# Kernel tuning notes

Measured on AMD Instinct MI355X. Metric: run time of the kernel, lower is better.

Reference implementation:

```python
import jax, jax.numpy as jnp
import numpy as np

N = 50000
E = 800000
T = 12
HID = 128
K = 3
F_IN = 7  # 1 (x) + 4 (env) + 2 (coords)
CIN = F_IN + HID  # DCRNN concatenates input with hidden state


def setup_inputs() -> dict:
    key = jax.random.key(0)
    ks = jax.random.split(key, 16)
    inp = {
        "x": jax.random.normal(ks[0], (N, T), dtype=jnp.float32),
        "env": jax.random.normal(ks[1], (N, 4, T), dtype=jnp.float32),
        "coords": jax.random.uniform(ks[2], (N, 2), dtype=jnp.float32),
        "edge_index": jax.random.randint(ks[3], (2, E), 0, N, dtype=jnp.int32),
        "edge_weight": jax.random.uniform(ks[4], (E,), dtype=jnp.float32),
        "local_night": jax.random.uniform(ks[5], (N, T + 1), dtype=jnp.float32),
        # DCRNN gate diffusion-conv weights: [2 (out/in direction), K, Cin, Cout]
        "Wz": jax.random.normal(ks[6], (2, K, CIN, HID), dtype=jnp.float32) * 0.05,
        "bz": jnp.zeros((HID,), dtype=jnp.float32),
        "Wr": jax.random.normal(ks[7], (2, K, CIN, HID), dtype=jnp.float32) * 0.05,
        "br": jnp.zeros((HID,), dtype=jnp.float32),
        "Wh": jax.random.normal(ks[8], (2, K, CIN, HID), dtype=jnp.float32) * 0.05,
        "bh": jnp.zeros((HID,), dtype=jnp.float32),
        "lin_W": jax.random.normal(ks[9], (HID, 1), dtype=jnp.float32) * 0.05,
        "lin_b": jnp.zeros((1,), dtype=jnp.float32),
    }
    return inp


def reference(x, env, coords, edge_weight, local_night, Wz, bz, Wr, br, Wh, bh, lin_W, lin_b, edge_index):
    row, col = edge_index[0], edge_index[1]
    n = x.shape[0]

    # out/in degrees of the weighted adjacency A[row, col] = w
    deg_out = jax.ops.segment_sum(edge_weight, row, num_segments=n)
    deg_in = jax.ops.segment_sum(edge_weight, col, num_segments=n)
    inv_out = jnp.where(deg_out > 0, 1.0 / deg_out, 0.0)
    inv_in = jnp.where(deg_in > 0, 1.0 / deg_in, 0.0)

    def prop_out(v):  # (D_O^{-1} A) v : gather from col, scatter-add to row
        msg = edge_weight[:, None] * v[col]
        return inv_out[:, None] * jax.ops.segment_sum(msg, row, num_segments=n)

    def prop_in(v):  # (D_I^{-1} A^T) v : gather from row, scatter-add to col
        msg = edge_weight[:, None] * v[row]
        return inv_in[:, None] * jax.ops.segment_sum(msg, col, num_segments=n)

    def dconv(X, W, b):
        # K-hop bidirectional diffusion convolution
        H = X @ (W[0, 0] + W[1, 0])
        Tx0 = X
        Tx_o = prop_out(X)
        Tx_i = prop_in(X)
        H = H + Tx_o @ W[0, 1] + Tx_i @ W[1, 1]
        for k in range(2, W.shape[1]):
            Tx_o = 2.0 * prop_out(Tx_o) - Tx0
            Tx_i = 2.0 * prop_in(Tx_i) - Tx0
            H = H + Tx_o @ W[0, k] + Tx_i @ W[1, k]
        return H + b

    env_t = jnp.moveaxis(env, -1, 0)          # [T, N, 4]
    night_t = jnp.transpose(local_night[:, 1:])  # [T, N]
    hid0 = jnp.zeros((n, HID), dtype=x.dtype)   # hidden state resets each call (H=None)

    def step(x_prev, ts):
        e, night = ts
        X = jnp.concatenate([x_prev, e, coords], axis=1)   # [N, 7]
        Xh = jnp.concatenate([X, hid0], axis=1)            # [N, 7+HID]
        Z = jax.nn.sigmoid(dconv(Xh, Wz, bz))
        R = jax.nn.sigmoid(dconv(Xh, Wr, br))  # H*R = 0 since H0 = 0; kept for fidelity
        H_tilde = jnp.tanh(dconv(Xh, Wh, bh))
        H_new = Z * hid0 + (1.0 - Z) * H_tilde
        out = jax.nn.relu(H_new) @ lin_W + lin_b           # [N, 1]
        out = out * night[:, None]
        return out, out

    x0 = x[:, 0:1]
    _, preds = jax.lax.scan(step, x0, (env_t, night_t))    # preds: [T, N, 1]
    predictions = jnp.concatenate([x0, jnp.transpose(preds[..., 0])], axis=1)  # [N, T+1]
    return predictions
```

## Files before the change

kernel.cpp:

```cpp
#include <hip/hip_runtime.h>
#include <hip/hip_fp16.h>

#define Nn 50000
#define Ee 800000
#define Tt 12
#define NBAND 8
#define BAND 6250
#define SCB 196

__global__ __launch_bounds__(256) void pack_hist_kernel(
    const int* __restrict__ ei, const float* __restrict__ ew,
    uint2* __restrict__ packed, int* __restrict__ cntR, int* __restrict__ cntC)
{
    int e = blockIdx.x * 256 + threadIdx.x;
    if (e >= Ee) return;
    int r = ei[e], c = ei[Ee + e];
    unsigned wb = __half_as_ushort(__float2half(ew[e]));
    packed[e] = make_uint2(((unsigned)c << 16) | wb, ((unsigned)r << 16) | wb);
    atomicAdd(&cntR[r], 1);
    atomicAdd(&cntC[c], 1);
}

__global__ __launch_bounds__(256) void scanA_kernel(
    const int* __restrict__ cntR, const int* __restrict__ cntC,
    int* __restrict__ bsum)
{
    const int* cnt = blockIdx.y ? cntC : cntR;
    int i = blockIdx.x * 256 + threadIdx.x;
    int v = (i < Nn) ? cnt[i] : 0;
    __shared__ int ws_[4];
    v += __shfl_xor(v, 1);  v += __shfl_xor(v, 2);  v += __shfl_xor(v, 4);
    v += __shfl_xor(v, 8);  v += __shfl_xor(v, 16); v += __shfl_xor(v, 32);
    if ((threadIdx.x & 63) == 0) ws_[threadIdx.x >> 6] = v;
    __syncthreads();
    if (threadIdx.x == 0)
        bsum[blockIdx.y * 256 + blockIdx.x] = ws_[0] + ws_[1] + ws_[2] + ws_[3];
}

__global__ __launch_bounds__(256) void scanB_kernel(
    const int* __restrict__ bsum, int* __restrict__ bbase)
{
    int y = blockIdx.x;
    __shared__ int s[256];
    int t = threadIdx.x;
    int v = (t < SCB) ? bsum[y * 256 + t] : 0;
    s[t] = v;
    __syncthreads();
    for (int off = 1; off < 256; off <<= 1) {
        int u = (t >= off) ? s[t - off] : 0;
        __syncthreads();
        s[t] += u;
        __syncthreads();
    }
    bbase[y * 256 + t] = s[t] - v;
}

__global__ __launch_bounds__(256) void scanC_kernel(
    const int* __restrict__ cntR, const int* __restrict__ cntC,
    const int* __restrict__ bbase,
    int* __restrict__ startR, int* __restrict__ startC,
    int* __restrict__ nextR, int* __restrict__ nextC)
{
    int y = blockIdx.y;
    const int* cnt = y ? cntC : cntR;
    int* start     = y ? startC : startR;
    int* nxt       = y ? nextC : nextR;
    int i = blockIdx.x * 256 + threadIdx.x;
    int v = (i < Nn) ? cnt[i] : 0;
    __shared__ int s[256];
    int t = threadIdx.x;
    s[t] = v;
    __syncthreads();
    for (int off = 1; off < 256; off <<= 1) {
        int u = (t >= off) ? s[t - off] : 0;
        __syncthreads();
        s[t] += u;
        __syncthreads();
    }
    int st = bbase[y * 256 + blockIdx.x] + s[t] - v;
    if (i < Nn) { start[i] = st; nxt[i] = st; }
}

__global__ __launch_bounds__(256) void scatter_banded(
    const uint2* __restrict__ packed,
    int* __restrict__ nextR, int* __restrict__ nextC,
    unsigned* __restrict__ adjR, unsigned* __restrict__ adjC)
{
    int band = blockIdx.x & (NBAND - 1);
    int chunk = blockIdx.x >> 3;
    int lo = band * BAND, hi = lo + BAND;
    int stride = (gridDim.x >> 3) * 256;
    for (int e = chunk * 256 + threadIdx.x; e < Ee; e += stride) {
        uint2 p = packed[e];
        int c = (int)(p.x >> 16);
        int r = (int)(p.y >> 16);
        if (r >= lo && r < hi) adjR[atomicAdd(&nextR[r], 1)] = p.x;
        if (c >= lo && c < hi) adjC[atomicAdd(&nextC[c], 1)] = p.y;
    }
}

__global__ __launch_bounds__(256) void weff_kernel(
    const float* __restrict__ Wz, const float* __restrict__ Wh,
    const float* __restrict__ bz, const float* __restrict__ bh,
    float* __restrict__ wzT, float* __restrict__ whT)
{
    int idx = blockIdx.x * 256 + threadIdx.x;
    if (idx >= 2 * 36 * 128) return;
    const float* W = (idx < 36 * 128) ? Wz : Wh;
    const float* B = (idx < 36 * 128) ? bz : bh;
    float* O       = (idx < 36 * 128) ? wzT : whT;
    int rem = idx % (36 * 128);
    int k = rem / 128, j = rem % 128;
    float v;
    if (k == 35) v = B[j];
    else {
        int p = k / 7, rr = k % 7;
        if (p == 0)      v = W[(0 * 135 + rr) * 128 + j] + W[(3 * 135 + rr) * 128 + j];
        else if (p == 1) v = W[(1 * 135 + rr) * 128 + j];
        else if (p == 2) v = W[(4 * 135 + rr) * 128 + j];
        else if (p == 3) v = W[(2 * 135 + rr) * 128 + j];
        else             v = W[(5 * 135 + rr) * 128 + j];
    }
    O[k * 128 + j] = v;
}

__global__ __launch_bounds__(256) void init_kernel(
    const float* __restrict__ x, const float* __restrict__ env,
    const float* __restrict__ coords, __half* __restrict__ Xh,
    float* __restrict__ out)
{
    int i = blockIdx.x * 256 + threadIdx.x;
    if (i >= Nn) return;
    float xv = x[i * Tt];
    __half* r = Xh + (long)i * 8;
    r[0] = __float2half(xv);
    #pragma unroll
    for (int c = 0; c < 4; c++) r[1 + c] = __float2half(env[i * 48 + c * 12]);
    r[5] = __float2half(coords[i * 2 + 0]);
    r[6] = __float2half(coords[i * 2 + 1]);
    r[7] = __half(0.f);
    out[i * 13 + 0] = xv;
}

__device__ __forceinline__ void unpack8(const __half* p, float* v) {
    uint4 hv = *((const uint4*)p);
    float2 p0 = __half22float2(*(__half2*)&hv.x);
    float2 p1 = __half22float2(*(__half2*)&hv.y);
    float2 p2 = __half22float2(*(__half2*)&hv.z);
    float2 p3 = __half22float2(*(__half2*)&hv.w);
    v[0] = p0.x; v[1] = p0.y; v[2] = p1.x; v[3] = p1.y;
    v[4] = p2.x; v[5] = p2.y; v[6] = p3.x;
}

__device__ __forceinline__ void pack8(__half* p, const float* v) {
    __half2 q0 = __floats2half2_rn(v[0], v[1]);
    __half2 q1 = __floats2half2_rn(v[2], v[3]);
    __half2 q2 = __floats2half2_rn(v[4], v[5]);
    __half2 q3 = __floats2half2_rn(v[6], 0.f);
    uint4 st;
    st.x = *(unsigned*)&q0; st.y = *(unsigned*)&q1;
    st.z = *(unsigned*)&q2; st.w = *(unsigned*)&q3;
    *((uint4*)p) = st;
}

__device__ __forceinline__ void acc7(float* a, float w, uint4 hv) {
    float2 p0 = __half22float2(*(__half2*)&hv.x);
    float2 p1 = __half22float2(*(__half2*)&hv.y);
    float2 p2 = __half22float2(*(__half2*)&hv.z);
    float2 p3 = __half22float2(*(__half2*)&hv.w);
    a[0] = fmaf(w, p0.x, a[0]); a[1] = fmaf(w, p0.y, a[1]);
    a[2] = fmaf(w, p1.x, a[2]); a[3] = fmaf(w, p1.y, a[3]);
    a[4] = fmaf(w, p2.x, a[4]); a[5] = fmaf(w, p2.y, a[5]);
    a[6] = fmaf(w, p3.x, a[6]);
}

__device__ __forceinline__ float wdec(unsigned ed) {
    return __half2float(__ushort_as_half((unsigned short)(ed & 0xffffu)));
}

__global__ __launch_bounds__(256) void gather1_kernel(
    const int* __restrict__ startR, const int* __restrict__ cntR,
    const unsigned* __restrict__ adjR,
    const int* __restrict__ startC, const int* __restrict__ cntC,
    const unsigned* __restrict__ adjC,
    const __half* __restrict__ Xh,
    __half* __restrict__ TxoH, __half* __restrict__ TxiH,
    float* __restrict__ inv_out, float* __restrict__ inv_in)
{
    int tid = blockIdx.x * 256 + threadIdx.x;
    if (tid >= Nn * 8) return;
    int node = tid >> 3;
    int dir = (tid >> 2) & 1, sub = tid & 3;
    const int*      st  = dir ? startC : startR;
    const int*      cn  = dir ? cntC : cntR;
    const unsigned* adj = dir ? adjC : adjR;
    int b = st[node], e = b + cn[node];
    float a[7] = {0.f, 0.f, 0.f, 0.f, 0.f, 0.f, 0.f};
    float sw = 0.f;
    int k = b + sub;
    for (; k + 12 < e; k += 16) {
        unsigned e0 = adj[k], e1 = adj[k + 4], e2 = adj[k + 8], e3 = adj[k + 12];
        uint4 r0 = *(const uint4*)(Xh + (long)(e0 >> 16) * 8);
        uint4 r1 = *(const uint4*)(Xh + (long)(e1 >> 16) * 8);
        uint4 r2 = *(const uint4*)(Xh + (long)(e2 >> 16) * 8);
        uint4 r3 = *(const uint4*)(Xh + (long)(e3 >> 16) * 8);
        float w0 = wdec(e0), w1 = wdec(e1), w2 = wdec(e2), w3 = wdec(e3);
        acc7(a, w0, r0); acc7(a, w1, r1); acc7(a, w2, r2); acc7(a, w3, r3);
        sw += (w0 + w1) + (w2 + w3);
    }
    for (; k < e; k += 4) {
        unsigned ed = adj[k];
        uint4 rv = *(const uint4*)(Xh + (long)(ed >> 16) * 8);
        float w = wdec(ed);
        acc7(a, w, rv);
        sw += w;
    }
    #pragma unroll
    for (int m = 1; m <= 2; m <<= 1) {
        #pragma unroll
        for (int q = 0; q < 7; q++) a[q] += __shfl_xor(a[q], m);
        sw += __shfl_xor(sw, m);
    }
    if (sub == 0) {
        float inv = sw > 0.f ? 1.f / sw : 0.f;
        (dir ? inv_in : inv_out)[node] = inv;
        #pragma unroll
        for (int q = 0; q < 7; q++) a[q] *= inv;
        pack8((dir ? TxiH : TxoH) + (long)node * 8, a);
    }
}

__global__ __launch_bounds__(256) void step2_kernel(
    const int* __restrict__ startR, const int* __restrict__ cntR,
    const unsigned* __restrict__ adjR,
    const int* __restrict__ startC, const int* __restrict__ cntC,
    const unsigned* __restrict__ adjC,
    const float* __restrict__ inv_out, const float* __restrict__ inv_in,
    const float* __restrict__ env, const float* __restrict__ night,
    const float* __restrict__ wzT, const float* __restrict__ whT,
    const float* __restrict__ linW, const float* __restrict__ linb,
    __half* __restrict__ Xh,
    const __half* __restrict__ TxoH, const __half* __restrict__ TxiH,
    float* __restrict__ out, int t)
{
    __shared__ float f_s[32][36];
    __shared__ float part_s[2][32];
    int tid = threadIdx.x;
    int base = blockIdx.x * 32;

    {
        int nl = tid >> 3;
        int dir = (tid >> 2) & 1, sub = tid & 3;
        int node = base + nl;
        int nc = node < Nn ? node : Nn - 1;
        const int*      st  = dir ? startC : startR;
        const int*      cn  = dir ? cntC : cntR;
        const unsigned* adj = dir ? adjC : adjR;
        const __half*   src = dir ? TxiH : TxoH;
        int b = st[nc], e = b + cn[nc];
        float a[7] = {0.f, 0.f, 0.f, 0.f, 0.f, 0.f, 0.f};
        int k = b + sub;
        for (; k + 12 < e; k += 16) {
            unsigned e0 = adj[k], e1 = adj[k + 4], e2 = adj[k + 8], e3 = adj[k + 12];
            uint4 r0 = *(const uint4*)(src + (long)(e0 >> 16) * 8);
            uint4 r1 = *(const uint4*)(src + (long)(e1 >> 16) * 8);
            uint4 r2 = *(const uint4*)(src + (long)(e2 >> 16) * 8);
            uint4 r3 = *(const uint4*)(src + (long)(e3 >> 16) * 8);
            float w0 = wdec(e0), w1 = wdec(e1), w2 = wdec(e2), w3 = wdec(e3);
            acc7(a, w0, r0); acc7(a, w1, r1); acc7(a, w2, r2); acc7(a, w3, r3);
        }
        for (; k < e; k += 4) {
            unsigned ed = adj[k];
            uint4 rv = *(const uint4*)(src + (long)(ed >> 16) * 8);
            acc7(a, wdec(ed), rv);
        }
        #pragma unroll
        for (int m = 1; m <= 2; m <<= 1) {
            #pragma unroll
            for (int q = 0; q < 7; q++) a[q] += __shfl_xor(a[q], m);
        }
        if (sub == 0) {
            float s2 = 2.f * (dir ? inv_in[nc] : inv_out[nc]);
            float xv[7], tx[7];
            unpack8(Xh + (long)nc * 8, xv);
            unpack8(src + (long)nc * 8, tx);
            #pragma unroll
            for (int q = 0; q < 7; q++) {
                f_s[nl][21 + 7 * dir + q] = fmaf(s2, a[q], -xv[q]);
                f_s[nl][7 + 7 * dir + q]  = tx[q];
            }
            if (dir == 0) {
                #pragma unroll
                for (int q = 0; q < 7; q++) f_s[nl][q] = xv[q];
                f_s[nl][35] = 1.f;
            }
        }
    }
    __syncthreads();

    int lane = tid & 63;
    int wave = tid >> 6;
    int chSel = wave & 1;
    int ch = chSel * 64 + lane;
    int half_id = wave >> 1;
    float wz[36], wh[36];
    #pragma unroll
    for (int k = 0; k < 36; k++) wz[k] = wzT[k * 128 + ch];
    #pragma unroll
    for (int k = 0; k < 36; k++) wh[k] = whT[k * 128 + ch];
    float lw = linW[ch];
    float lb = linb[0];

    #pragma unroll 1
    for (int n = 0; n < 16; n++) {
        int ni = half_id * 16 + n;
        const float4* fv = (const float4*)f_s[ni];
        float hz = 0.f, hh = 0.f;
        #pragma unroll
        for (int q = 0; q < 9; q++) {
            float4 fq = fv[q];
            hz = fmaf(fq.x, wz[q*4+0], hz); hh = fmaf(fq.x, wh[q*4+0], hh);
            hz = fmaf(fq.y, wz[q*4+1], hz); hh = fmaf(fq.y, wh[q*4+1], hh);
            hz = fmaf(fq.z, wz[q*4+2], hz); hh = fmaf(fq.z, wh[q*4+2], hh);
            hz = fmaf(fq.w, wz[q*4+3], hz); hh = fmaf(fq.w, wh[q*4+3], hh);
        }
        float z  = 1.f / (1.f + __expf(-hz));
        float e2 = __expf(2.f * hh);
        float ht = 1.f - 2.f / (e2 + 1.f);
        float v = fmaxf((1.f - z) * ht, 0.f) * lw;
        v += __shfl_xor(v, 1);  v += __shfl_xor(v, 2);  v += __shfl_xor(v, 4);
        v += __shfl_xor(v, 8);  v += __shfl_xor(v, 16); v += __shfl_xor(v, 32);
        if (lane == 0) part_s[chSel][ni] = v;
    }
    __syncthreads();
    if (tid < 32) {
        int node = base + tid;
        if (node < Nn) {
            float o = part_s[0][tid] + part_s[1][tid] + lb;
            o *= night[(long)node * 13 + t + 1];
            out[(long)node * 13 + t + 1] = o;
            if (t + 1 < Tt) {
                __half* xr = Xh + (long)node * 8;
                xr[0] = __float2half(o);
                #pragma unroll
                for (int c = 0; c < 4; c++)
                    xr[1 + c] = __float2half(env[(long)node * 48 + c * 12 + t + 1]);
            }
        }
    }
}

extern "C" void kernel_launch(void* const* d_in, const int* in_sizes, int n_in,
                              void* d_out, int out_size, void* d_ws, size_t ws_size,
                              hipStream_t stream) {
    const float* x      = (const float*)d_in[0];
    const float* env    = (const float*)d_in[1];
    const float* coords = (const float*)d_in[2];
    const int*   ei     = (const int*)d_in[3];
    const float* ew     = (const float*)d_in[4];
    const float* night  = (const float*)d_in[5];
    const float* Wz     = (const float*)d_in[6];
    const float* bz     = (const float*)d_in[7];
    const float* Wh     = (const float*)d_in[10];
    const float* bh     = (const float*)d_in[11];
    const float* linW   = (const float*)d_in[12];
    const float* linb   = (const float*)d_in[13];
    float* out = (float*)d_out;

    float* w = (float*)d_ws;
    float* wzT     = w;
    float* whT     = w + 4608;
    float* inv_out = w + 9216;
    float* inv_in  = w + 59216;
    __half* Xh   = (__half*)(w + 109216);
    __half* TxoH = (__half*)(w + 309216);
    __half* TxiH = (__half*)(w + 509216);
    int* cntR    = (int*)(w + 709216);
    int* cntC    = cntR + 50000;
    int* startR  = cntC + 50000;
    int* startC  = startR + 50000;
    int* nextR   = startC + 50000;
    int* nextC   = nextR + 50000;
    int* bsum    = nextC + 50000;
    int* bbase   = bsum + 512;
    uint2* packed  = (uint2*)(bbase + 512);
    unsigned* adjR = (unsigned*)(packed + Ee);
    unsigned* adjC = adjR + Ee;

    hipMemsetAsync(cntR, 0, 2 * Nn * sizeof(int), stream);
    pack_hist_kernel<<<(Ee + 255) / 256, 256, 0, stream>>>(ei, ew, packed, cntR, cntC);
    scanA_kernel<<<dim3(SCB, 2), 256, 0, stream>>>(cntR, cntC, bsum);
    scanB_kernel<<<2, 256, 0, stream>>>(bsum, bbase);
    scanC_kernel<<<dim3(SCB, 2), 256, 0, stream>>>(
        cntR, cntC, bbase, startR, startC, nextR, nextC);
    scatter_banded<<<8 * 256, 256, 0, stream>>>(packed, nextR, nextC, adjR, adjC);

    weff_kernel<<<(2 * 36 * 128 + 255) / 256, 256, 0, stream>>>(Wz, Wh, bz, bh, wzT, whT);
    init_kernel<<<(Nn + 255) / 256, 256, 0, stream>>>(x, env, coords, Xh, out);

    for (int t = 0; t < Tt; t++) {
        gather1_kernel<<<(Nn * 8 + 255) / 256, 256, 0, stream>>>(
            startR, cntR, adjR, startC, cntC, adjC, Xh, TxoH, TxiH, inv_out, inv_in);
        step2_kernel<<<(Nn + 31) / 32, 256, 0, stream>>>(
            startR, cntR, adjR, startC, cntC, adjC, inv_out, inv_in,
            env, night, wzT, whT, linW, linb, Xh, TxoH, TxiH, out, t);
    }
}
```

Before: 788.2 us.

## Build CSR with deterministic chunked histograms and fuse timestep loop into cooperative kernel

Graph preprocessing switches from global-atomic counting and scattering to a two-pass scheme. Per-chunk, per-band shared-memory histograms feed the prefix scan, and a second pass places edges using shared-memory cursors. The separate packed edge buffer is dropped. The 24 per-timestep kernel launches are replaced by one persistent cooperative kernel that loops over timesteps with grid-wide syncs, trading launch overhead for grid-barrier cost and a smaller resident grid. Adjacency reads use nontemporal loads.

```diff
diff --git a/kernel.cpp b/kernel.cpp
--- a/kernel.cpp
+++ b/kernel.cpp
@@ -1,40 +1,61 @@
 #include <hip/hip_runtime.h>
 #include <hip/hip_fp16.h>
+#include <hip/hip_cooperative_groups.h>
+
+namespace cg = cooperative_groups;
 
 #define Nn 50000
 #define Ee 800000
 #define Tt 12
 #define NBAND 8
 #define BAND 6250
+#define NCH 16
+#define CHSZ 50000
 #define SCB 196
-
-__global__ __launch_bounds__(256) void pack_hist_kernel(
-    const int* __restrict__ ei, const float* __restrict__ ew,
-    uint2* __restrict__ packed, int* __restrict__ cntR, int* __restrict__ cntC)
-{
-    int e = blockIdx.x * 256 + threadIdx.x;
-    if (e >= Ee) return;
-    int r = ei[e], c = ei[Ee + e];
-    unsigned wb = __half_as_ushort(__float2half(ew[e]));
-    packed[e] = make_uint2(((unsigned)c << 16) | wb, ((unsigned)r << 16) | wb);
-    atomicAdd(&cntR[r], 1);
-    atomicAdd(&cntC[c], 1);
+#define NCHUNK2 1563
+
+__global__ __launch_bounds__(256) void pass1_kernel(
+    const int* __restrict__ ei, int* __restrict__ cntCh)
+{
+    __shared__ int hR[BAND], hC[BAND];
+    int j = blockIdx.x >> 3;
+    int b = blockIdx.x & 7;
+    int lo = b * BAND;
+    for (int i = threadIdx.x; i < BAND; i += 256) { hR[i] = 0; hC[i] = 0; }
+    __syncthreads();
+    int e0 = j * CHSZ;
+    for (int e = e0 + threadIdx.x; e < e0 + CHSZ; e += 256) {
+        int r = __builtin_nontemporal_load(ei + e);
+        int c = __builtin_nontemporal_load(ei + Ee + e);
+        if ((unsigned)(r - lo) < BAND) atomicAdd(&hR[r - lo], 1);
+        if ((unsigned)(c - lo) < BAND) atomicAdd(&hC[c - lo], 1);
+    }
+    __syncthreads();
+    for (int i = threadIdx.x; i < BAND; i += 256) {
+        cntCh[(0 * NCH + j) * Nn + lo + i] = hR[i];
+        cntCh[(1 * NCH + j) * Nn + lo + i] = hC[i];
+    }
 }
 
 __global__ __launch_bounds__(256) void scanA_kernel(
-    const int* __restrict__ cntR, const int* __restrict__ cntC,
-    int* __restrict__ bsum)
-{
-    const int* cnt = blockIdx.y ? cntC : cntR;
+    const int* __restrict__ cntCh, int* __restrict__ tot, int* __restrict__ bsum)
+{
+    int y = blockIdx.y;
     int i = blockIdx.x * 256 + threadIdx.x;
-    int v = (i < Nn) ? cnt[i] : 0;
+    int v = 0;
+    if (i < Nn) {
+        #pragma unroll
+        for (int j = 0; j < NCH; j++) v += cntCh[(y * NCH + j) * Nn + i];
+        tot[y * Nn + i] = v;
+    }
     __shared__ int ws_[4];
-    v += __shfl_xor(v, 1);  v += __shfl_xor(v, 2);  v += __shfl_xor(v, 4);
-    v += __shfl_xor(v, 8);  v += __shfl_xor(v, 16); v += __shfl_xor(v, 32);
-    if ((threadIdx.x & 63) == 0) ws_[threadIdx.x >> 6] = v;
+    int s = v;
+    s += __shfl_xor(s, 1);  s += __shfl_xor(s, 2);  s += __shfl_xor(s, 4);
+    s += __shfl_xor(s, 8);  s += __shfl_xor(s, 16); s += __shfl_xor(s, 32);
+    if ((threadIdx.x & 63) == 0) ws_[threadIdx.x >> 6] = s;
     __syncthreads();
     if (threadIdx.x == 0)
-        bsum[blockIdx.y * 256 + blockIdx.x] = ws_[0] + ws_[1] + ws_[2] + ws_[3];
+        bsum[y * 256 + blockIdx.x] = ws_[0] + ws_[1] + ws_[2] + ws_[3];
 }
 
 __global__ __launch_bounds__(256) void scanB_kernel(
@@ -56,17 +77,12 @@
 }
 
 __global__ __launch_bounds__(256) void scanC_kernel(
-    const int* __restrict__ cntR, const int* __restrict__ cntC,
-    const int* __restrict__ bbase,
-    int* __restrict__ startR, int* __restrict__ startC,
-    int* __restrict__ nextR, int* __restrict__ nextC)
+    const int* __restrict__ tot, const int* __restrict__ bbase,
+    int* __restrict__ start)
 {
     int y = blockIdx.y;
-    const int* cnt = y ? cntC : cntR;
-    int* start     = y ? startC : startR;
-    int* nxt       = y ? nextC : nextR;
     int i = blockIdx.x * 256 + threadIdx.x;
-    int v = (i < Nn) ? cnt[i] : 0;
+    int v = (i < Nn) ? tot[y * Nn + i] : 0;
     __shared__ int s[256];
     int t = threadIdx.x;
     s[t] = v;
@@ -77,25 +93,42 @@
         s[t] += u;
         __syncthreads();
     }
-    int st = bbase[y * 256 + blockIdx.x] + s[t] - v;
-    if (i < Nn) { start[i] = st; nxt[i] = st; }
-}
-
-__global__ __launch_bounds__(256) void scatter_banded(
-    const uint2* __restrict__ packed,
-    int* __restrict__ nextR, int* __restrict__ nextC,
+    if (i < Nn) start[y * Nn + i] = bbase[y * 256 + blockIdx.x] + s[t] - v;
+}
+
+__global__ __launch_bounds__(256) void pass2_kernel(
+    const int* __restrict__ ei, const float* __restrict__ ew,
+    const int* __restrict__ cntCh, const int* __restrict__ start,
     unsigned* __restrict__ adjR, unsigned* __restrict__ adjC)
 {
-    int band = blockIdx.x & (NBAND - 1);
-    int chunk = blockIdx.x >> 3;
-    int lo = band * BAND, hi = lo + BAND;
-    int stride = (gridDim.x >> 3) * 256;
-    for (int e = chunk * 256 + threadIdx.x; e < Ee; e += stride) {
-        uint2 p = packed[e];
-        int c = (int)(p.x >> 16);
-        int r = (int)(p.y >> 16);
-        if (r >= lo && r < hi) adjR[atomicAdd(&nextR[r], 1)] = p.x;
-        if (c >= lo && c < hi) adjC[atomicAdd(&nextC[c], 1)] = p.y;
+    __shared__ int curR[BAND], curC[BAND];
+    int j = blockIdx.x >> 3;
+    int b = blockIdx.x & 7;
+    int lo = b * BAND;
+    for (int i = threadIdx.x; i < BAND; i += 256) {
+        int sR = start[lo + i];
+        int sC = start[Nn + lo + i];
+        for (int jj = 0; jj < j; jj++) {
+            sR += cntCh[(0 * NCH + jj) * Nn + lo + i];
+            sC += cntCh[(1 * NCH + jj) * Nn + lo + i];
+        }
+        curR[i] = sR; curC[i] = sC;
+    }
+    __syncthreads();
+    int e0 = j * CHSZ;
+    for (int e = e0 + threadIdx.x; e < e0 + CHSZ; e += 256) {
+        int r = __builtin_nontemporal_load(ei + e);
+        int c = __builtin_nontemporal_load(ei + Ee + e);
+        float wf = __builtin_nontemporal_load(ew + e);
+        unsigned wb = __half_as_ushort(__float2half(wf));
+        if ((unsigned)(r - lo) < BAND) {
+            int slot = atomicAdd(&curR[r - lo], 1);
+            adjR[slot] = ((unsigned)c << 16) | wb;
+        }
+        if ((unsigned)(c - lo) < BAND) {
+            int slot = atomicAdd(&curC[c - lo], 1);
+            adjC[slot] = ((unsigned)r << 16) | wb;
+        }
     }
 }
 
@@ -178,131 +211,29 @@
     return __half2float(__ushort_as_half((unsigned short)(ed & 0xffffu)));
 }
 
-__global__ __launch_bounds__(256) void gather1_kernel(
-    const int* __restrict__ startR, const int* __restrict__ cntR,
+__global__ __launch_bounds__(256) void loop_kernel(
+    const int* __restrict__ startR, const int* __restrict__ totR,
     const unsigned* __restrict__ adjR,
-    const int* __restrict__ startC, const int* __restrict__ cntC,
+    const int* __restrict__ startC, const int* __restrict__ totC,
     const unsigned* __restrict__ adjC,
-    const __half* __restrict__ Xh,
-    __half* __restrict__ TxoH, __half* __restrict__ TxiH,
-    float* __restrict__ inv_out, float* __restrict__ inv_in)
-{
-    int tid = blockIdx.x * 256 + threadIdx.x;
-    if (tid >= Nn * 8) return;
-    int node = tid >> 3;
-    int dir = (tid >> 2) & 1, sub = tid & 3;
-    const int*      st  = dir ? startC : startR;
-    const int*      cn  = dir ? cntC : cntR;
-    const unsigned* adj = dir ? adjC : adjR;
-    int b = st[node], e = b + cn[node];
-    float a[7] = {0.f, 0.f, 0.f, 0.f, 0.f, 0.f, 0.f};
-    float sw = 0.f;
-    int k = b + sub;
-    for (; k + 12 < e; k += 16) {
-        unsigned e0 = adj[k], e1 = adj[k + 4], e2 = adj[k + 8], e3 = adj[k + 12];
-        uint4 r0 = *(const uint4*)(Xh + (long)(e0 >> 16) * 8);
-        uint4 r1 = *(const uint4*)(Xh + (long)(e1 >> 16) * 8);
-        uint4 r2 = *(const uint4*)(Xh + (long)(e2 >> 16) * 8);
-        uint4 r3 = *(const uint4*)(Xh + (long)(e3 >> 16) * 8);
-        float w0 = wdec(e0), w1 = wdec(e1), w2 = wdec(e2), w3 = wdec(e3);
-        acc7(a, w0, r0); acc7(a, w1, r1); acc7(a, w2, r2); acc7(a, w3, r3);
-        sw += (w0 + w1) + (w2 + w3);
-    }
-    for (; k < e; k += 4) {
-        unsigned ed = adj[k];
-        uint4 rv = *(const uint4*)(Xh + (long)(ed >> 16) * 8);
-        float w = wdec(ed);
-        acc7(a, w, rv);
-        sw += w;
-    }
-    #pragma unroll
-    for (int m = 1; m <= 2; m <<= 1) {
-        #pragma unroll
-        for (int q = 0; q < 7; q++) a[q] += __shfl_xor(a[q], m);
-        sw += __shfl_xor(sw, m);
-    }
-    if (sub == 0) {
-        float inv = sw > 0.f ? 1.f / sw : 0.f;
-        (dir ? inv_in : inv_out)[node] = inv;
-        #pragma unroll
-        for (int q = 0; q < 7; q++) a[q] *= inv;
-        pack8((dir ? TxiH : TxoH) + (long)node * 8, a);
-    }
-}
-
-__global__ __launch_bounds__(256) void step2_kernel(
-    const int* __restrict__ startR, const int* __restrict__ cntR,
-    const unsigned* __restrict__ adjR,
-    const int* __restrict__ startC, const int* __restrict__ cntC,
-    const unsigned* __restrict__ adjC,
-    const float* __restrict__ inv_out, const float* __restrict__ inv_in,
+    float* __restrict__ inv_out, float* __restrict__ inv_in,
     const float* __restrict__ env, const float* __restrict__ night,
     const float* __restrict__ wzT, const float* __restrict__ whT,
     const float* __restrict__ linW, const float* __restrict__ linb,
-    __half* __restrict__ Xh,
-    const __half* __restrict__ TxoH, const __half* __restrict__ TxiH,
-    float* __restrict__ out, int t)
-{
+    __half* __restrict__ Xh, __half* __restrict__ TxoH, __half* __restrict__ TxiH,
+    float* __restrict__ out)
+{
+    cg::grid_group grid = cg::this_grid();
     __shared__ float f_s[32][36];
     __shared__ float part_s[2][32];
     int tid = threadIdx.x;
-    int base = blockIdx.x * 32;
-
-    {
-        int nl = tid >> 3;
-        int dir = (tid >> 2) & 1, sub = tid & 3;
-        int node = base + nl;
-        int nc = node < Nn ? node : Nn - 1;
-        const int*      st  = dir ? startC : startR;
-        const int*      cn  = dir ? cntC : cntR;
-        const unsigned* adj = dir ? adjC : adjR;
-        const __half*   src = dir ? TxiH : TxoH;
-        int b = st[nc], e = b + cn[nc];
-        float a[7] = {0.f, 0.f, 0.f, 0.f, 0.f, 0.f, 0.f};
-        int k = b + sub;
-        for (; k + 12 < e; k += 16) {
-            unsigned e0 = adj[k], e1 = adj[k + 4], e2 = adj[k + 8], e3 = adj[k + 12];
-            uint4 r0 = *(const uint4*)(src + (long)(e0 >> 16) * 8);
-            uint4 r1 = *(const uint4*)(src + (long)(e1 >> 16) * 8);
-            uint4 r2 = *(const uint4*)(src + (long)(e2 >> 16) * 8);
-            uint4 r3 = *(const uint4*)(src + (long)(e3 >> 16) * 8);
-            float w0 = wdec(e0), w1 = wdec(e1), w2 = wdec(e2), w3 = wdec(e3);
-            acc7(a, w0, r0); acc7(a, w1, r1); acc7(a, w2, r2); acc7(a, w3, r3);
-        }
-        for (; k < e; k += 4) {
-            unsigned ed = adj[k];
-            uint4 rv = *(const uint4*)(src + (long)(ed >> 16) * 8);
-            acc7(a, wdec(ed), rv);
-        }
-        #pragma unroll
-        for (int m = 1; m <= 2; m <<= 1) {
-            #pragma unroll
-            for (int q = 0; q < 7; q++) a[q] += __shfl_xor(a[q], m);
-        }
-        if (sub == 0) {
-            float s2 = 2.f * (dir ? inv_in[nc] : inv_out[nc]);
-            float xv[7], tx[7];
-            unpack8(Xh + (long)nc * 8, xv);
-            unpack8(src + (long)nc * 8, tx);
-            #pragma unroll
-            for (int q = 0; q < 7; q++) {
-                f_s[nl][21 + 7 * dir + q] = fmaf(s2, a[q], -xv[q]);
-                f_s[nl][7 + 7 * dir + q]  = tx[q];
-            }
-            if (dir == 0) {
-                #pragma unroll
-                for (int q = 0; q < 7; q++) f_s[nl][q] = xv[q];
-                f_s[nl][35] = 1.f;
-            }
-        }
-    }
-    __syncthreads();
-
     int lane = tid & 63;
     int wave = tid >> 6;
     int chSel = wave & 1;
     int ch = chSel * 64 + lane;
     int half_id = wave >> 1;
+    int gsz = gridDim.x * 256;
+
     float wz[36], wh[36];
     #pragma unroll
     for (int k = 0; k < 36; k++) wz[k] = wzT[k * 128 + ch];
@@ -311,42 +242,149 @@
     float lw = linW[ch];
     float lb = linb[0];
 
-    #pragma unroll 1
-    for (int n = 0; n < 16; n++) {
-        int ni = half_id * 16 + n;
-        const float4* fv = (const float4*)f_s[ni];
-        float hz = 0.f, hh = 0.f;
-        #pragma unroll
-        for (int q = 0; q < 9; q++) {
-            float4 fq = fv[q];
-            hz = fmaf(fq.x, wz[q*4+0], hz); hh = fmaf(fq.x, wh[q*4+0], hh);
-            hz = fmaf(fq.y, wz[q*4+1], hz); hh = fmaf(fq.y, wh[q*4+1], hh);
-            hz = fmaf(fq.z, wz[q*4+2], hz); hh = fmaf(fq.z, wh[q*4+2], hh);
-            hz = fmaf(fq.w, wz[q*4+3], hz); hh = fmaf(fq.w, wh[q*4+3], hh);
+    for (int t = 0; t < Tt; t++) {
+        for (int task = blockIdx.x * 256 + tid; task < Nn * 8; task += gsz) {
+            int node = task >> 3;
+            int dir = (task >> 2) & 1, sub = task & 3;
+            const int*      st  = dir ? startC : startR;
+            const int*      to  = dir ? totC : totR;
+            const unsigned* adj = dir ? adjC : adjR;
+            int b = st[node], e = b + to[node];
+            float a[7] = {0.f, 0.f, 0.f, 0.f, 0.f, 0.f, 0.f};
+            float sw = 0.f;
+            int k = b + sub;
+            for (; k + 12 < e; k += 16) {
+                unsigned e0 = __builtin_nontemporal_load(adj + k);
+                unsigned e1 = __builtin_nontemporal_load(adj + k + 4);
+                unsigned e2 = __builtin_nontemporal_load(adj + k + 8);
+                unsigned e3 = __builtin_nontemporal_load(adj + k + 12);
+                uint4 r0 = *(const uint4*)(Xh + (long)(e0 >> 16) * 8);
+                uint4 r1 = *(const uint4*)(Xh + (long)(e1 >> 16) * 8);
+                uint4 r2 = *(const uint4*)(Xh + (long)(e2 >> 16) * 8);
+                uint4 r3 = *(const uint4*)(Xh + (long)(e3 >> 16) * 8);
+                float w0 = wdec(e0), w1 = wdec(e1), w2 = wdec(e2), w3 = wdec(e3);
+                acc7(a, w0, r0); acc7(a, w1, r1); acc7(a, w2, r2); acc7(a, w3, r3);
+                sw += (w0 + w1) + (w2 + w3);
+            }
+            for (; k < e; k += 4) {
+                unsigned ed = __builtin_nontemporal_load(adj + k);
+                uint4 rv = *(const uint4*)(Xh + (long)(ed >> 16) * 8);
+                float w = wdec(ed);
+                acc7(a, w, rv);
+                sw += w;
+            }
+            #pragma unroll
+            for (int m = 1; m <= 2; m <<= 1) {
+                #pragma unroll
+                for (int q = 0; q < 7; q++) a[q] += __shfl_xor(a[q], m);
+                sw += __shfl_xor(sw, m);
+            }
+            if (sub == 0) {
+                float inv = sw > 0.f ? 1.f / sw : 0.f;
+                (dir ? inv_in : inv_out)[node] = inv;
+                #pragma unroll
+                for (int q = 0; q < 7; q++) a[q] *= inv;
+                pack8((dir ? TxiH : TxoH) + (long)node * 8, a);
+            }
         }
-        float z  = 1.f / (1.f + __expf(-hz));
-        float e2 = __expf(2.f * hh);
-        float ht = 1.f - 2.f / (e2 + 1.f);
-        float v = fmaxf((1.f - z) * ht, 0.f) * lw;
-        v += __shfl_xor(v, 1);  v += __shfl_xor(v, 2);  v += __shfl_xor(v, 4);
-        v += __shfl_xor(v, 8);  v += __shfl_xor(v, 16); v += __shfl_xor(v, 32);
-        if (lane == 0) part_s[chSel][ni] = v;
-    }
-    __syncthreads();
-    if (tid < 32) {
-        int node = base + tid;
-        if (node < Nn) {
-            float o = part_s[0][tid] + part_s[1][tid] + lb;
-            o *= night[(long)node * 13 + t + 1];
-            out[(long)node * 13 + t + 1] = o;
-            if (t + 1 < Tt) {
-                __half* xr = Xh + (long)node * 8;
-                xr[0] = __float2half(o);
+        __threadfence();
+        grid.sync();
+
+        for (int chunk = blockIdx.x; chunk < NCHUNK2; chunk += gridDim.x) {
+            int base = chunk * 32;
+            {
+                int nl = tid >> 3;
+                int dir = (tid >> 2) & 1, sub = tid & 3;
+                int node = base + nl;
+                int nc = node < Nn ? node : Nn - 1;
+                const int*      st  = dir ? startC : startR;
+                const int*      to  = dir ? totC : totR;
+                const unsigned* adj = dir ? adjC : adjR;
+                const __half*   src = dir ? TxiH : TxoH;
+                int b = st[nc], e = b + to[nc];
+                float a[7] = {0.f, 0.f, 0.f, 0.f, 0.f, 0.f, 0.f};
+                int k = b + sub;
+                for (; k + 12 < e; k += 16) {
+                    unsigned e0 = __builtin_nontemporal_load(adj + k);
+                    unsigned e1 = __builtin_nontemporal_load(adj + k + 4);
+                    unsigned e2 = __builtin_nontemporal_load(adj + k + 8);
+                    unsigned e3 = __builtin_nontemporal_load(adj + k + 12);
+                    uint4 r0 = *(const uint4*)(src + (long)(e0 >> 16) * 8);
+                    uint4 r1 = *(const uint4*)(src + (long)(e1 >> 16) * 8);
+                    uint4 r2 = *(const uint4*)(src + (long)(e2 >> 16) * 8);
+                    uint4 r3 = *(const uint4*)(src + (long)(e3 >> 16) * 8);
+                    float w0 = wdec(e0), w1 = wdec(e1), w2 = wdec(e2), w3 = wdec(e3);
+                    acc7(a, w0, r0); acc7(a, w1, r1); acc7(a, w2, r2); acc7(a, w3, r3);
+                }
+                for (; k < e; k += 4) {
+                    unsigned ed = __builtin_nontemporal_load(adj + k);
+                    uint4 rv = *(const uint4*)(src + (long)(ed >> 16) * 8);
+                    acc7(a, wdec(ed), rv);
+                }
                 #pragma unroll
-                for (int c = 0; c < 4; c++)
-                    xr[1 + c] = __float2half(env[(long)node * 48 + c * 12 + t + 1]);
-            }
+                for (int m = 1; m <= 2; m <<= 1) {
+                    #pragma unroll
+                    for (int q = 0; q < 7; q++) a[q] += __shfl_xor(a[q], m);
+                }
+                if (sub == 0) {
+                    float s2 = 2.f * (dir ? inv_in[nc] : inv_out[nc]);
+                    float xv[7], tx[7];
+                    unpack8(Xh + (long)nc * 8, xv);
+                    unpack8(src + (long)nc * 8, tx);
+                    #pragma unroll
+                    for (int q = 0; q < 7; q++) {
+                        f_s[nl][21 + 7 * dir + q] = fmaf(s2, a[q], -xv[q]);
+                        f_s[nl][7 + 7 * dir + q]  = tx[q];
+                    }
+                    if (dir == 0) {
+                        #pragma unroll
+                        for (int q = 0; q < 7; q++) f_s[nl][q] = xv[q];
+                        f_s[nl][35] = 1.f;
+                    }
+                }
+            }
+            __syncthreads();
+            #pragma unroll 1
+            for (int n = 0; n < 16; n++) {
+                int ni = half_id * 16 + n;
+                const float4* fv = (const float4*)f_s[ni];
+                float hz = 0.f, hh = 0.f;
+                #pragma unroll
+                for (int q = 0; q < 9; q++) {
+                    float4 fq = fv[q];
+                    hz = fmaf(fq.x, wz[q*4+0], hz); hh = fmaf(fq.x, wh[q*4+0], hh);
+                    hz = fmaf(fq.y, wz[q*4+1], hz); hh = fmaf(fq.y, wh[q*4+1], hh);
+                    hz = fmaf(fq.z, wz[q*4+2], hz); hh = fmaf(fq.z, wh[q*4+2], hh);
+                    hz = fmaf(fq.w, wz[q*4+3], hz); hh = fmaf(fq.w, wh[q*4+3], hh);
+                }
+                float z  = 1.f / (1.f + __expf(-hz));
+                float e2 = __expf(2.f * hh);
+                float ht = 1.f - 2.f / (e2 + 1.f);
+                float v = fmaxf((1.f - z) * ht, 0.f) * lw;
+                v += __shfl_xor(v, 1);  v += __shfl_xor(v, 2);  v += __shfl_xor(v, 4);
+                v += __shfl_xor(v, 8);  v += __shfl_xor(v, 16); v += __shfl_xor(v, 32);
+                if (lane == 0) part_s[chSel][ni] = v;
+            }
+            __syncthreads();
+            if (tid < 32) {
+                int node = base + tid;
+                if (node < Nn) {
+                    float o = part_s[0][tid] + part_s[1][tid] + lb;
+                    o *= night[(long)node * 13 + t + 1];
+                    out[(long)node * 13 + t + 1] = o;
+                    if (t + 1 < Tt) {
+                        __half* xr = Xh + (long)node * 8;
+                        xr[0] = __float2half(o);
+                        #pragma unroll
+                        for (int c = 0; c < 4; c++)
+                            xr[1 + c] = __float2half(env[(long)node * 48 + c * 12 + t + 1]);
+                    }
+                }
+            }
+            __syncthreads();
         }
+        __threadfence();
+        grid.sync();
     }
 }
 
@@ -375,34 +413,40 @@
     __half* Xh   = (__half*)(w + 109216);
     __half* TxoH = (__half*)(w + 309216);
     __half* TxiH = (__half*)(w + 509216);
-    int* cntR    = (int*)(w + 709216);
-    int* cntC    = cntR + 50000;
-    int* startR  = cntC + 50000;
-    int* startC  = startR + 50000;
-    int* nextR   = startC + 50000;
-    int* nextC   = nextR + 50000;
-    int* bsum    = nextC + 50000;
-    int* bbase   = bsum + 512;
-    uint2* packed  = (uint2*)(bbase + 512);
-    unsigned* adjR = (unsigned*)(packed + Ee);
+    int* ibase   = (int*)(w + 709216);
+    int* tot     = ibase;
+    int* start   = ibase + 100000;
+    int* cntCh   = ibase + 200000;
+    int* bsum    = ibase + 1800000;
+    int* bbase   = ibase + 1800512;
+    unsigned* adjR = (unsigned*)(ibase + 1801024);
     unsigned* adjC = adjR + Ee;
 
-    hipMemsetAsync(cntR, 0, 2 * Nn * sizeof(int), stream);
-    pack_hist_kernel<<<(Ee + 255) / 256, 256, 0, stream>>>(ei, ew, packed, cntR, cntC);
-    scanA_kernel<<<dim3(SCB, 2), 256, 0, stream>>>(cntR, cntC, bsum);
+    pass1_kernel<<<NCH * NBAND, 256, 0, stream>>>(ei, cntCh);
+    scanA_kernel<<<dim3(SCB, 2), 256, 0, stream>>>(cntCh, tot, bsum);
     scanB_kernel<<<2, 256, 0, stream>>>(bsum, bbase);
-    scanC_kernel<<<dim3(SCB, 2), 256, 0, stream>>>(
-        cntR, cntC, bbase, startR, startC, nextR, nextC);
-    scatter_banded<<<8 * 256, 256, 0, stream>>>(packed, nextR, nextC, adjR, adjC);
+    scanC_kernel<<<dim3(SCB, 2), 256, 0, stream>>>(tot, bbase, start);
+    pass2_kernel<<<NCH * NBAND, 256, 0, stream>>>(ei, ew, cntCh, start, adjR, adjC);
 
     weff_kernel<<<(2 * 36 * 128 + 255) / 256, 256, 0, stream>>>(Wz, Wh, bz, bh, wzT, whT);
     init_kernel<<<(Nn + 255) / 256, 256, 0, stream>>>(x, env, coords, Xh, out);
 
-    for (int t = 0; t < Tt; t++) {
-        gather1_kernel<<<(Nn * 8 + 255) / 256, 256, 0, stream>>>(
-            startR, cntR, adjR, startC, cntC, adjC, Xh, TxoH, TxiH, inv_out, inv_in);
-        step2_kernel<<<(Nn + 31) / 32, 256, 0, stream>>>(
-            startR, cntR, adjR, startC, cntC, adjC, inv_out, inv_in,
-            env, night, wzT, whT, linW, linb, Xh, TxoH, TxiH, out, t);
-    }
-}
+    int nb = 0;
+    hipError_t oe = hipOccupancyMaxActiveBlocksPerMultiprocessor(&nb, loop_kernel, 256, 0);
+    if (oe != hipSuccess || nb < 1) nb = 2;
+    int G = nb * 256;
+    if (G > NCHUNK2) G = NCHUNK2;
+
+    const int* startR = start;
+    const int* startC = start + Nn;
+    const int* totR   = tot;
+    const int* totC   = tot + Nn;
+    void* kargs[] = {
+        (void*)&startR, (void*)&totR, (void*)&adjR,
+        (void*)&startC, (void*)&totC, (void*)&adjC,
+        (void*)&inv_out, (void*)&inv_in,
+        (void*)&env, (void*)&night,
+        (void*)&wzT, (void*)&whT, (void*)&linW, (void*)&linb,
+        (void*)&Xh, (void*)&TxoH, (void*)&TxiH, (void*)&out };
+    hipLaunchCooperativeKernel(loop_kernel, dim3(G), dim3(256), kargs, 0, stream);
+}
```

Result: slower. 2.965 ms (+276.2%).
